# Optimization experiments

Hardware: AMD Instinct MI355X
Metric: run time of the kernel (lower is better)

Reference implementation:

```python
import jax, jax.numpy as jnp
import numpy as np

EPS = 1e-5

def _layernorm(x, g, b):
    m = jnp.mean(x, axis=-1, keepdims=True)
    v = jnp.var(x, axis=-1, keepdims=True)
    return (x - m) * jax.lax.rsqrt(v + EPS) * g + b

def setup_inputs() -> dict:
    key = jax.random.key(0)
    ks = jax.random.split(key, 8)
    B, N, D, H = 4, 2048, 1024, 16
    F = 2 * D
    s = 0.02
    return {
        "x": jax.random.normal(ks[0], (B, N, D), jnp.float32),
        "mask": jnp.zeros((B, N, N), jnp.float32),
        "Wq": jax.random.normal(ks[1], (D, D), jnp.float32) * s,
        "Wk": jax.random.normal(ks[2], (D, D), jnp.float32) * s,
        "Wv": jax.random.normal(ks[3], (D, D), jnp.float32) * s,
        "Wc": jax.random.normal(ks[4], (D, D), jnp.float32) * s,
        "bc": jnp.zeros((D,), jnp.float32),
        "W1": jax.random.normal(ks[5], (D, F), jnp.float32) * s,
        "b1": jnp.zeros((F,), jnp.float32),
        "W2": jax.random.normal(ks[6], (F, D), jnp.float32) * s,
        "b2": jnp.zeros((D,), jnp.float32),
        "g1": jnp.ones((D,), jnp.float32),
        "be1": jnp.zeros((D,), jnp.float32),
        "g2": jnp.ones((D,), jnp.float32),
        "be2": jnp.zeros((D,), jnp.float32),
    }

def reference(x, mask, Wq, Wk, Wv, Wc, bc, W1, b1, W2, b2, g1, be1, g2, be2):
    B, N, D = x.shape
    H = 16
    Dh = D // H
    scale = 1.0 / np.sqrt(Dh).astype(np.float32)
    # projections -> [B, H, N, Dh]
    def heads(t):
        return t.reshape(B, N, H, Dh).transpose(0, 2, 1, 3)
    q = heads(x @ Wq)
    k = heads(x @ Wk)
    v = heads(x @ Wv)
    score = jnp.einsum('bhnd,bhmd->bhnm', q, k) * scale + mask[:, None, :, :]
    attn = jnp.einsum('bhnm,bhmd->bhnd', jax.nn.softmax(score, axis=-1), v)
    attn = attn.transpose(0, 2, 1, 3).reshape(B, N, D)
    x = x + attn @ Wc + bc
    x = _layernorm(x, g1, be1)
    x = x + jnp.maximum(x @ W1 + b1, 0.0) @ W2 + b2
    x = _layernorm(x, g2, be2)
    return x
```

## Files before the change

### kernel.cpp

```cpp
#include <hip/hip_runtime.h>
#include <hip/hip_bf16.h>


#define DEV __device__ __forceinline__

using s16x8  = __attribute__((ext_vector_type(8))) short;
using f32x4  = __attribute__((ext_vector_type(4))) float;

DEV unsigned short f2bf(float f) {
  unsigned u = __float_as_uint(f);
  u += 0x7fffu + ((u >> 16) & 1u);
  return (unsigned short)(u >> 16);
}
DEV unsigned cvt_pk_bf16(float lo, float hi) {
  unsigned r;
  asm("v_cvt_pk_bf16_f32 %0, %1, %2" : "=v"(r) : "v"(lo), "v"(hi));
  return r;
}
DEV float bf2f(unsigned short b) { return __uint_as_float((unsigned)b << 16); }

typedef __attribute__((address_space(3))) unsigned lds_u32_t;
typedef const __attribute__((address_space(1))) unsigned glb_u32_t;

DEV void gld_lds16(const void* g, void* l) {
  __builtin_amdgcn_global_load_lds((glb_u32_t*)g, (lds_u32_t*)l, 16, 0, 0);
}

template<int RELU, int VOUT>
__global__ __launch_bounds__(512, 2)
void gemm8p(const unsigned short* __restrict__ A, const unsigned short* __restrict__ Bt,
            unsigned short* __restrict__ Cb, const float* __restrict__ bias,
            unsigned short* __restrict__ vtout, int M, int N, int K)
{
  __shared__ unsigned short Sh[2][2][256 * 64];
  const int tid = threadIdx.x;
  const int w = tid >> 6, lane = tid & 63;
  const int g = lane >> 4, q = lane & 15;
  const int wr = w >> 2, wc = w & 3;

  const int nwg  = gridDim.x * gridDim.y;
  const int flat = blockIdx.y * gridDim.x + blockIdx.x;
  const int rm   = (flat & 7) * (nwg >> 3) + (flat >> 3);
  const int m0 = (rm / gridDim.x) * 256, n0 = (rm % gridDim.x) * 256;

  f32x4 acc[8][4] = {};

  const int srow = w * 8 + (lane >> 3);
  const int scol = ((lane & 7) ^ (lane >> 3)) * 8;
  const unsigned short* Ag = A  + (size_t)(m0 + srow) * K + scol;
  const unsigned short* Bg = Bt + (size_t)(n0 + srow) * K + scol;

  auto STG = [&](const unsigned short* Gb, int buf, int ab, int half, int kt) {
    const unsigned short* gs = Gb + (size_t)(half * 128) * K + kt * 64;
    unsigned short* ls = &Sh[buf][ab][(half * 128 + w * 8) * 64];
    gld_lds16(gs, ls);
    gld_lds16(gs + (size_t)64 * K, ls + 64 * 64);
  };
  auto LDA = [&](int buf, int mq, s16x8 af[4][2]) {
#pragma unroll
    for (int mm = 0; mm < 4; ++mm) {
      const unsigned short* rp = &Sh[buf][0][(wr * 128 + mq * 64 + mm * 16 + q) * 64];
#pragma unroll
      for (int kk = 0; kk < 2; ++kk)
        af[mm][kk] = *(const s16x8*)(rp + (((kk * 4 + g) ^ (q & 7)) * 8));
    }
  };
  auto LDB = [&](int buf, int nq, s16x8 bf[2][2]) {
#pragma unroll
    for (int nn = 0; nn < 2; ++nn) {
      const unsigned short* rp = &Sh[buf][1][(wc * 64 + nq * 32 + nn * 16 + q) * 64];
#pragma unroll
      for (int kk = 0; kk < 2; ++kk)
        bf[nn][kk] = *(const s16x8*)(rp + (((kk * 4 + g) ^ (q & 7)) * 8));
    }
  };
  auto MQ = [&](int mq, int nq, const s16x8 af[4][2], const s16x8 bf[2][2]) {
    __builtin_amdgcn_s_setprio(1);
#pragma unroll
    for (int kk = 0; kk < 2; ++kk)
#pragma unroll
      for (int mm = 0; mm < 4; ++mm)
#pragma unroll
        for (int nn = 0; nn < 2; ++nn)
          acc[mq * 4 + mm][nq * 2 + nn] = __builtin_amdgcn_mfma_f32_16x16x32_bf16(
              af[mm][kk], bf[nn][kk], acc[mq * 4 + mm][nq * 2 + nn], 0, 0, 0);
    __builtin_amdgcn_s_setprio(0);
  };
  auto BAR = [&]() { __builtin_amdgcn_sched_barrier(0); __builtin_amdgcn_s_barrier(); };

  STG(Ag, 0, 0, 0, 0); STG(Ag, 0, 0, 1, 0);
  STG(Bg, 0, 1, 0, 0); STG(Bg, 0, 1, 1, 0);

  const int NKT = K >> 6;
  s16x8 af[4][2], bf0[2][2], bf1[2][2];
#pragma unroll 1
  for (int kt = 0; kt < NKT; ++kt) {
    const int b = kt & 1, sb = b ^ 1, kn = kt + 1;
    const bool stg = (kn < NKT);
    if (stg) { STG(Ag, sb, 0, 0, kn); asm volatile("s_waitcnt vmcnt(2)" ::: "memory"); }
    else     {                        asm volatile("s_waitcnt vmcnt(0)" ::: "memory"); }
    BAR();
    LDA(b, 0, af); LDB(b, 0, bf0);
    MQ(0, 0, af, bf0);
    BAR();
    if (stg) STG(Ag, sb, 0, 1, kn);
    LDB(b, 1, bf1);
    MQ(0, 1, af, bf1);
    BAR();
    if (stg) STG(Bg, sb, 1, 0, kn);
    LDA(b, 1, af);
    MQ(1, 0, af, bf0);
    BAR();
    if (stg) STG(Bg, sb, 1, 1, kn);
    MQ(1, 1, af, bf1);
    BAR();
  }

#pragma unroll
  for (int n = 0; n < 4; ++n) {
    const int col = n0 + wc * 64 + n * 16 + q;
    if (VOUT && col >= 2048) {
      const int cv = col - 2048;
#pragma unroll
      for (int m = 0; m < 8; ++m) {
        const int row0 = m0 + wr * 128 + m * 16 + g * 4;
        const int bb = row0 >> 11;
        ushort4 pk;
        pk.x = f2bf(acc[m][n][0]); pk.y = f2bf(acc[m][n][1]);
        pk.z = f2bf(acc[m][n][2]); pk.w = f2bf(acc[m][n][3]);
        *(ushort4*)(vtout + ((size_t)bb * 1024 + cv) * 2048 + (row0 & 2047)) = pk;
      }
    } else {
      const float scl = (VOUT && col < 1024) ? 0.18033688011112042f : 1.0f;
      const float bv = bias ? bias[col] : 0.0f;
#pragma unroll
      for (int m = 0; m < 8; ++m) {
        const int row0 = m0 + wr * 128 + m * 16 + g * 4;
#pragma unroll
        for (int r = 0; r < 4; ++r) {
          float v = acc[m][n][r] * scl + bv;
          if (RELU) v = fmaxf(v, 0.0f);
          Cb[(size_t)(row0 + r) * N + col] = f2bf(v);
        }
      }
    }
  }
}

template<int RELU, int RESID, int OUTF>
__global__ __launch_bounds__(256)
void gemm_bt(const unsigned short* __restrict__ A, const unsigned short* __restrict__ Bt,
             unsigned short* __restrict__ Cb, float* __restrict__ Cf,
             const float* __restrict__ bias, const float* __restrict__ resid,
             const unsigned short* __restrict__ residb,
             int M, int N, int K)
{
  __shared__ unsigned short As[2][4096];
  __shared__ unsigned short Bs[2][4096];
  const int tid  = threadIdx.x;
  const int wave = tid >> 6, lane = tid & 63;
  const int g = lane >> 4, q = lane & 15;

  const int nwg  = gridDim.x * gridDim.y;
  const int flat = blockIdx.y * gridDim.x + blockIdx.x;
  const int rm   = (nwg & 7) ? flat : ((flat & 7) * (nwg >> 3) + (flat >> 3));
  const int m0 = (rm / gridDim.x) * 128, n0 = (rm % gridDim.x) * 128;
  const int wr = wave >> 1, wc = wave & 1;

  f32x4 acc[4][4] = {};

  const int i0 = wave * 512 + lane * 8;
  const int i1 = 2048 + i0;

  auto STAGE = [&](int buf, int kt) {
    gld_lds16(A  + (size_t)(m0 + (i0 >> 5)) * K + kt + (i0 & 31), As[buf] + wave * 512);
    gld_lds16(Bt + (size_t)(n0 + (i0 >> 5)) * K + kt + (i0 & 31), Bs[buf] + wave * 512);
    gld_lds16(A  + (size_t)(m0 + (i1 >> 5)) * K + kt + (i1 & 31), As[buf] + 2048 + wave * 512);
    gld_lds16(Bt + (size_t)(n0 + (i1 >> 5)) * K + kt + (i1 & 31), Bs[buf] + 2048 + wave * 512);
  };

  STAGE(0, 0);
  __syncthreads();
  int cur = 0;
#pragma unroll 1
  for (int kt = 0; kt < K; kt += 32) {
    if (kt + 32 < K) STAGE(cur ^ 1, kt + 32);
    s16x8 a[4], b[4];
#pragma unroll
    for (int m = 0; m < 4; ++m)
      a[m] = *(const s16x8*)(As[cur] + (wr * 64 + m * 16 + q) * 32 + g * 8);
#pragma unroll
    for (int n = 0; n < 4; ++n)
      b[n] = *(const s16x8*)(Bs[cur] + (wc * 64 + n * 16 + q) * 32 + g * 8);
    __builtin_amdgcn_s_setprio(1);
#pragma unroll
    for (int m = 0; m < 4; ++m)
#pragma unroll
      for (int n = 0; n < 4; ++n)
        acc[m][n] = __builtin_amdgcn_mfma_f32_16x16x32_bf16(a[m], b[n], acc[m][n], 0, 0, 0);
    __builtin_amdgcn_s_setprio(0);
    __syncthreads();
    cur ^= 1;
  }

#pragma unroll
  for (int n = 0; n < 4; ++n) {
    const int col = n0 + wc * 64 + n * 16 + q;
    const float bv = bias ? bias[col] : 0.0f;
#pragma unroll
    for (int m = 0; m < 4; ++m) {
      const int row0 = m0 + wr * 64 + m * 16 + g * 4;
#pragma unroll
      for (int r = 0; r < 4; ++r) {
        float v = acc[m][n][r] + bv;
        if (RELU) v = fmaxf(v, 0.0f);
        if (RESID == 1) v += resid[(size_t)(row0 + r) * N + col];
        if (RESID == 2) v += bf2f(residb[(size_t)(row0 + r) * N + col]);
        if (OUTF) Cf[(size_t)(row0 + r) * N + col] = v;
        else      Cb[(size_t)(row0 + r) * N + col] = f2bf(v);
      }
    }
  }
}

__global__ __launch_bounds__(256, 4)
void attn_kernel(const unsigned short* __restrict__ qkv,
                 const unsigned short* __restrict__ vt,
                 const float* __restrict__ mask,
                 unsigned short* __restrict__ outb)
{
  __shared__ unsigned short Ks[2][4096];
  __shared__ unsigned short Vs[2][4096];
  __shared__ unsigned short Pl[4][1024];
  const int tid = threadIdx.x, wave = tid >> 6, lane = tid & 63;
  const int g = lane >> 4, q = lane & 15;

  const int flat = blockIdx.y * 32 + blockIdx.x;
  const int rm   = (flat & 7) * 256 + (flat >> 3);
  const int h  = rm & 15;
  const int qt = (rm >> 4) & 31;
  const int b  = rm >> 9;
  const int qrow = qt * 64 + wave * 16;
  const size_t tok0 = (size_t)b * 2048;

  const unsigned short* Qp = qkv + (tok0 + qrow + q) * 3072 + h * 64;
  const s16x8 bq0 = *(const s16x8*)(Qp + g * 8);
  const s16x8 bq1 = *(const s16x8*)(Qp + 32 + g * 8);
  const float* Mp = mask + ((size_t)b * 2048 + qrow + q) * 2048 + g * 4;

  const int lr = lane >> 3;
  const int sc = (lane & 7) ^ lr;
  const unsigned short* Kg = qkv + tok0 * 3072 + 1024 + h * 64
                           + (size_t)(wave * 16 + lr) * 3072 + sc * 8;
  const unsigned short* Vg = vt + (((size_t)b * 16 + h) * 64 + wave * 16 + lr) * 2048 + sc * 8;
  unsigned short* KsW = Ks[0] + wave * 1024;
  unsigned short* VsW = Vs[0] + wave * 1024;

  s16x8 ones;
#pragma unroll
  for (int j = 0; j < 8; ++j) ones[j] = (short)0x3F80;

  f32x4 ot[4] = {};
  f32x4 sacc = {};
  f32x4 mk0[4], mk1[4];
  char* Pw = (char*)&Pl[wave][0];
  const float L2E = 1.4426950408889634f;

  gld_lds16(Kg,            KsW);
  gld_lds16(Kg + 8 * 3072, KsW + 512);
  gld_lds16(Vg,            VsW);
  gld_lds16(Vg + 8 * 2048, VsW + 512);
#pragma unroll
  for (int m2 = 0; m2 < 4; ++m2) {
    const f32x4 r = *(const f32x4*)(Mp + m2 * 16);
#pragma unroll
    for (int i = 0; i < 4; ++i) mk0[m2][i] = fmaf(r[i], L2E, -8.0f);
  }
  __syncthreads();

#define ATTN_TILE(BUF, MKC, MKN, STG)                                          \
  {                                                                            \
    f32x4 mu[4];                                                               \
    if (STG) {                                                                 \
      Kg += 64 * 3072; Vg += 64; Mp += 64;                                     \
      gld_lds16(Kg,            KsW + (BUF ^ 1) * 4096);                        \
      gld_lds16(Kg + 8 * 3072, KsW + (BUF ^ 1) * 4096 + 512);                  \
      gld_lds16(Vg,            VsW + (BUF ^ 1) * 4096);                        \
      gld_lds16(Vg + 8 * 2048, VsW + (BUF ^ 1) * 4096 + 512);                  \
      mu[0] = *(const f32x4*)(Mp);      mu[1] = *(const f32x4*)(Mp + 16);      \
      mu[2] = *(const f32x4*)(Mp + 32); mu[3] = *(const f32x4*)(Mp + 48);      \
    }                                                                          \
    __builtin_amdgcn_s_setprio(1);                                             \
    _Pragma("unroll")                                                          \
    for (int m2 = 0; m2 < 4; ++m2) {                                           \
      const unsigned short* kp = Ks[BUF] + (m2 * 16 + q) * 64;                 \
      const s16x8 ak0 = *(const s16x8*)(kp + ((g       ^ (q & 7)) * 8));       \
      const s16x8 ak1 = *(const s16x8*)(kp + (((g + 4) ^ (q & 7)) * 8));       \
      MKC[m2] = __builtin_amdgcn_mfma_f32_16x16x32_bf16(ak0, bq0, MKC[m2], 0, 0, 0); \
      MKC[m2] = __builtin_amdgcn_mfma_f32_16x16x32_bf16(ak1, bq1, MKC[m2], 0, 0, 0); \
    }                                                                          \
    __builtin_amdgcn_s_setprio(0);                                             \
    _Pragma("unroll")                                                          \
    for (int m2 = 0; m2 < 4; ++m2) {                                           \
      MKC[m2][0] = exp2f(MKC[m2][0]); MKC[m2][1] = exp2f(MKC[m2][1]);          \
      MKC[m2][2] = exp2f(MKC[m2][2]); MKC[m2][3] = exp2f(MKC[m2][3]);          \
      const int bir  = m2 * 32 + g * 8;                                        \
      const int addr = q * 128 + (((bir >> 4) ^ (q & 7)) << 4) + (bir & 15);   \
      uint2 pk;                                                                \
      pk.x = cvt_pk_bf16(MKC[m2][0], MKC[m2][1]);                              \
      pk.y = cvt_pk_bf16(MKC[m2][2], MKC[m2][3]);                              \
      *(uint2*)(Pw + addr) = pk;                                               \
    }                                                                          \
    __builtin_amdgcn_s_setprio(1);                                             \
    _Pragma("unroll")                                                          \
    for (int kb = 0; kb < 2; ++kb) {                                           \
      const int blk = (kb * 4 + g) ^ (q & 7);                                  \
      const s16x8 pb = *(const s16x8*)(Pw + q * 128 + blk * 16);               \
      sacc = __builtin_amdgcn_mfma_f32_16x16x32_bf16(ones, pb, sacc, 0, 0, 0); \
      _Pragma("unroll")                                                        \
      for (int mm = 0; mm < 4; ++mm) {                                         \
        const s16x8 av = *(const s16x8*)(Vs[BUF] + (mm * 16 + q) * 64 + blk * 8); \
        ot[mm] = __builtin_amdgcn_mfma_f32_16x16x32_bf16(av, pb, ot[mm], 0, 0, 0); \
      }                                                                        \
    }                                                                          \
    __builtin_amdgcn_s_setprio(0);                                             \
    if (STG) {                                                                 \
      _Pragma("unroll")                                                        \
      for (int m2 = 0; m2 < 4; ++m2) {                                         \
        MKN[m2][0] = fmaf(mu[m2][0], L2E, -8.0f);                              \
        MKN[m2][1] = fmaf(mu[m2][1], L2E, -8.0f);                              \
        MKN[m2][2] = fmaf(mu[m2][2], L2E, -8.0f);                              \
        MKN[m2][3] = fmaf(mu[m2][3], L2E, -8.0f);                              \
      }                                                                        \
    }                                                                          \
    __syncthreads();                                                           \
  }

#pragma unroll 1
  for (int tt = 0; tt < 16; ++tt) {
    ATTN_TILE(0, mk0, mk1, true);
    ATTN_TILE(1, mk1, mk0, (tt < 15));
  }
#undef ATTN_TILE

  const float inv = 1.0f / sacc[0];
#pragma unroll
  for (int mm = 0; mm < 4; ++mm) {
    const int bir  = mm * 32 + g * 8;
    const int addr = q * 128 + (((bir >> 4) ^ (q & 7)) << 4) + (bir & 15);
    uint2 pk;
    pk.x = cvt_pk_bf16(ot[mm][0] * inv, ot[mm][1] * inv);
    pk.y = cvt_pk_bf16(ot[mm][2] * inv, ot[mm][3] * inv);
    *(uint2*)(Pw + addr) = pk;
  }
#pragma unroll
  for (int p = 0; p < 2; ++p) {
    const int c  = p * 64 + lane;
    const int qq = c >> 3, cc = c & 7;
    const int blk = cc ^ (qq & 7);
    const s16x8 vv = *(const s16x8*)(Pw + qq * 128 + blk * 16);
    *(s16x8*)(outb + (tok0 + qrow + qq) * 1024 + h * 64 + cc * 8) = vv;
  }
}

template<int INBF>
__global__ __launch_bounds__(256)
void ln_kernel(const float* __restrict__ inf, const unsigned short* __restrict__ inb,
               float* __restrict__ outf, unsigned short* __restrict__ outb,
               const float* __restrict__ gam, const float* __restrict__ bet)
{
  __shared__ float red[8];
  const int row = blockIdx.x, tid = threadIdx.x;
  f32x4 v;
  if (INBF) {
    const uint2 u = *(const uint2*)(inb + (size_t)row * 1024 + tid * 4);
    v[0] = __uint_as_float(u.x << 16); v[1] = __uint_as_float(u.x & 0xffff0000u);
    v[2] = __uint_as_float(u.y << 16); v[3] = __uint_as_float(u.y & 0xffff0000u);
  } else {
    v = *(const f32x4*)(inf + (size_t)row * 1024 + tid * 4);
  }
  float s  = v[0] + v[1] + v[2] + v[3];
  float ss = v[0]*v[0] + v[1]*v[1] + v[2]*v[2] + v[3]*v[3];
#pragma unroll
  for (int o = 1; o < 64; o <<= 1) { s += __shfl_xor(s, o); ss += __shfl_xor(ss, o); }
  if ((tid & 63) == 0) { red[tid >> 6] = s; red[4 + (tid >> 6)] = ss; }
  __syncthreads();
  s  = red[0] + red[1] + red[2] + red[3];
  ss = red[4] + red[5] + red[6] + red[7];
  const float mean = s * (1.0f / 1024.0f);
  const float var  = ss * (1.0f / 1024.0f) - mean * mean;
  const float rstd = rsqrtf(var + 1e-5f);
  const f32x4 gm = *(const f32x4*)(gam + tid * 4);
  const f32x4 bt = *(const f32x4*)(bet + tid * 4);
  f32x4 o;
#pragma unroll
  for (int j = 0; j < 4; ++j) o[j] = (v[j] - mean) * rstd * gm[j] + bt[j];
  if (outf) *(f32x4*)(outf + (size_t)row * 1024 + tid * 4) = o;
  if (outb) {
    uint2 pk; pk.x = cvt_pk_bf16(o[0], o[1]); pk.y = cvt_pk_bf16(o[2], o[3]);
    *(uint2*)(outb + (size_t)row * 1024 + tid * 4) = pk;
  }
}

__global__ __launch_bounds__(256)
void prep_kernel(const float* __restrict__ x, unsigned short* __restrict__ xb,
                 const float* __restrict__ Wq, const float* __restrict__ Wk,
                 const float* __restrict__ Wv, const float* __restrict__ Wc,
                 const float* __restrict__ W1, const float* __restrict__ W2,
                 unsigned short* __restrict__ wqkvt, unsigned short* __restrict__ wct,
                 unsigned short* __restrict__ w1t, unsigned short* __restrict__ w2t)
{
  const int bid = blockIdx.x;
  if (bid < 8192) {
    const size_t i = ((size_t)bid * 256 + threadIdx.x) * 4;
    const f32x4 v = *(const f32x4*)(x + i);
    uint2 pk; pk.x = cvt_pk_bf16(v[0], v[1]); pk.y = cvt_pk_bf16(v[2], v[3]);
    *(uint2*)(xb + i) = pk;
    return;
  }
  __shared__ float t[32][33];
  const int t2 = bid - 8192;
  const float* in; unsigned short* out; int R, C, bx, by;
  if (t2 < 4096) {
    const int widx = t2 >> 10, sub = t2 & 1023;
    in  = (widx == 0) ? Wq : (widx == 1) ? Wk : (widx == 2) ? Wv : Wc;
    out = (widx < 3) ? (wqkvt + (size_t)widx * 1024 * 1024) : wct;
    R = 1024; C = 1024; bx = sub & 31; by = sub >> 5;
  } else if (t2 < 6144) {
    const int sub = t2 - 4096;
    in = W1; out = w1t; R = 1024; C = 2048; bx = sub & 63; by = sub >> 6;
  } else {
    const int sub = t2 - 6144;
    in = W2; out = w2t; R = 2048; C = 1024; bx = sub & 31; by = sub >> 5;
  }
  const int tx = threadIdx.x & 31, ty = threadIdx.x >> 5;
  const int c0 = bx * 32, r0 = by * 32;
#pragma unroll
  for (int k = 0; k < 4; ++k)
    t[ty + k * 8][tx] = in[(size_t)(r0 + ty + k * 8) * C + c0 + tx];
  __syncthreads();
#pragma unroll
  for (int k = 0; k < 4; ++k)
    out[(size_t)(c0 + ty + k * 8) * R + r0 + tx] = f2bf(t[tx][ty + k * 8]);
}

extern "C" void kernel_launch(void* const* d_in, const int* in_sizes, int n_in,
                              void* d_out, int out_size, void* d_ws, size_t ws_size,
                              hipStream_t stream)
{
  (void)in_sizes; (void)n_in; (void)out_size; (void)ws_size;
  const float* x   = (const float*)d_in[0];
  const float* msk = (const float*)d_in[1];
  const float* Wq  = (const float*)d_in[2];
  const float* Wk  = (const float*)d_in[3];
  const float* Wv  = (const float*)d_in[4];
  const float* Wc  = (const float*)d_in[5];
  const float* bc  = (const float*)d_in[6];
  const float* W1  = (const float*)d_in[7];
  const float* b1  = (const float*)d_in[8];
  const float* W2  = (const float*)d_in[9];
  const float* b2  = (const float*)d_in[10];
  const float* g1  = (const float*)d_in[11];
  const float* be1 = (const float*)d_in[12];
  const float* g2  = (const float*)d_in[13];
  const float* be2 = (const float*)d_in[14];
  float* out = (float*)d_out;
  char* ws = (char*)d_ws;
  const size_t MB = 1u << 20;
  unsigned short* xb    = (unsigned short*)(ws + 0 * MB);
  unsigned short* wqkvt = (unsigned short*)(ws + 16 * MB);
  unsigned short* wct   = (unsigned short*)(ws + 22 * MB);
  unsigned short* w1t   = (unsigned short*)(ws + 24 * MB);
  unsigned short* w2t   = (unsigned short*)(ws + 28 * MB);
  unsigned short* qkv   = (unsigned short*)(ws + 32 * MB);
  unsigned short* vt    = (unsigned short*)(ws + 80 * MB);
  unsigned short* attnb = (unsigned short*)(ws + 96 * MB);
  unsigned short* y1b   = (unsigned short*)(ws + 112 * MB);
  unsigned short* h1b   = (unsigned short*)(ws + 128 * MB);
  unsigned short* midb  = (unsigned short*)(ws + 32 * MB);
  unsigned short* z2b   = (unsigned short*)(ws + 64 * MB);

  prep_kernel<<<16384, 256, 0, stream>>>(x, xb, Wq, Wk, Wv, Wc, W1, W2,
                                         wqkvt, wct, w1t, w2t);
  gemm8p<0, 1><<<dim3(12, 32), 512, 0, stream>>>(xb, wqkvt, qkv, nullptr, vt,
                                                 8192, 3072, 1024);
  attn_kernel<<<dim3(32, 64), 256, 0, stream>>>(qkv, vt, msk, attnb);
  gemm_bt<0, 2, 0><<<dim3(8, 64), 256, 0, stream>>>(attnb, wct, y1b, nullptr,
                                                    bc, nullptr, xb, 8192, 1024, 1024);
  ln_kernel<1><<<8192, 256, 0, stream>>>(nullptr, y1b, nullptr, h1b, g1, be1);
  gemm8p<1, 0><<<dim3(8, 32), 512, 0, stream>>>(h1b, w1t, midb, b1, nullptr,
                                                8192, 2048, 1024);
  gemm_bt<0, 2, 0><<<dim3(8, 64), 256, 0, stream>>>(midb, w2t, z2b, nullptr,
                                                    b2, nullptr, h1b, 8192, 1024, 2048);
  ln_kernel<1><<<8192, 256, 0, stream>>>(nullptr, z2b, out, nullptr, g2, be2);
}
```

Baseline: 407.2 us.

## Split-K the second FFN GEMM onto the 256-tile kernel, fuse reduction into LayerNorm

The W2 GEMM (K=2048, N=1024) moves from the smaller-tile gemm_bt kernel to the 256x256 gemm8p kernel with a two-way split over K. Each half writes fp32 partials, which gives 256 workgroups instead of 128 big tiles. The final LayerNorm now sums the two partials and adds bias and the bf16 residual before normalising, so the separate epilogue pass goes away. In exchange the code writes and reads two fp32 partial buffers of 32MB each, instead of one bf16 output.

```diff
diff --git a/kernel.cpp b/kernel.cpp
--- a/kernel.cpp
+++ b/kernel.cpp
@@ -26,11 +26,12 @@
   __builtin_amdgcn_global_load_lds((glb_u32_t*)g, (lds_u32_t*)l, 16, 0, 0);
 }
 
-template<int RELU, int VOUT>
+template<int RELU, int VOUT, int SPLITK>
 __global__ __launch_bounds__(512, 2)
 void gemm8p(const unsigned short* __restrict__ A, const unsigned short* __restrict__ Bt,
             unsigned short* __restrict__ Cb, const float* __restrict__ bias,
-            unsigned short* __restrict__ vtout, int M, int N, int K)
+            unsigned short* __restrict__ vtout, float* __restrict__ Cf,
+            int M, int N, int K)
 {
   __shared__ unsigned short Sh[2][2][256 * 64];
   const int tid = threadIdx.x;
@@ -41,14 +42,21 @@
   const int nwg  = gridDim.x * gridDim.y;
   const int flat = blockIdx.y * gridDim.x + blockIdx.x;
   const int rm   = (flat & 7) * (nwg >> 3) + (flat >> 3);
-  const int m0 = (rm / gridDim.x) * 256, n0 = (rm % gridDim.x) * 256;
+  int m0, n0, kz = 0;
+  if (SPLITK) {
+    kz = rm >> 7;
+    const int sp = rm & 127;
+    m0 = (sp >> 2) * 256; n0 = (sp & 3) * 256;
+  } else {
+    m0 = (rm / gridDim.x) * 256; n0 = (rm % gridDim.x) * 256;
+  }
 
   f32x4 acc[8][4] = {};
 
   const int srow = w * 8 + (lane >> 3);
   const int scol = ((lane & 7) ^ (lane >> 3)) * 8;
-  const unsigned short* Ag = A  + (size_t)(m0 + srow) * K + scol;
-  const unsigned short* Bg = Bt + (size_t)(n0 + srow) * K + scol;
+  const unsigned short* Ag = A  + (size_t)(m0 + srow) * K + scol + (SPLITK ? kz * (K >> 1) : 0);
+  const unsigned short* Bg = Bt + (size_t)(n0 + srow) * K + scol + (SPLITK ? kz * (K >> 1) : 0);
 
   auto STG = [&](const unsigned short* Gb, int buf, int ab, int half, int kt) {
     const unsigned short* gs = Gb + (size_t)(half * 128) * K + kt * 64;
@@ -91,7 +99,7 @@
   STG(Ag, 0, 0, 0, 0); STG(Ag, 0, 0, 1, 0);
   STG(Bg, 0, 1, 0, 0); STG(Bg, 0, 1, 1, 0);
 
-  const int NKT = K >> 6;
+  const int NKT = SPLITK ? (K >> 7) : (K >> 6);
   s16x8 af[4][2], bf0[2][2], bf1[2][2];
 #pragma unroll 1
   for (int kt = 0; kt < NKT; ++kt) {
@@ -119,7 +127,16 @@
 #pragma unroll
   for (int n = 0; n < 4; ++n) {
     const int col = n0 + wc * 64 + n * 16 + q;
-    if (VOUT && col >= 2048) {
+    if (SPLITK) {
+      float* Cp = Cf + (size_t)kz * M * N;
+#pragma unroll
+      for (int m = 0; m < 8; ++m) {
+        const int row0 = m0 + wr * 128 + m * 16 + g * 4;
+#pragma unroll
+        for (int r = 0; r < 4; ++r)
+          Cp[(size_t)(row0 + r) * N + col] = acc[m][n][r];
+      }
+    } else if (VOUT && col >= 2048) {
       const int cv = col - 2048;
 #pragma unroll
       for (int m = 0; m < 8; ++m) {
@@ -214,7 +231,6 @@
       for (int r = 0; r < 4; ++r) {
         float v = acc[m][n][r] + bv;
         if (RELU) v = fmaxf(v, 0.0f);
-        if (RESID == 1) v += resid[(size_t)(row0 + r) * N + col];
         if (RESID == 2) v += bf2f(residb[(size_t)(row0 + r) * N + col]);
         if (OUTF) Cf[(size_t)(row0 + r) * N + col] = v;
         else      Cb[(size_t)(row0 + r) * N + col] = f2bf(v);
@@ -363,21 +379,31 @@
   }
 }
 
-template<int INBF>
+template<int MODE>
 __global__ __launch_bounds__(256)
-void ln_kernel(const float* __restrict__ inf, const unsigned short* __restrict__ inb,
+void ln_kernel(const unsigned short* __restrict__ inb,
+               const float* __restrict__ p0, const float* __restrict__ p1,
+               const float* __restrict__ bias, const unsigned short* __restrict__ residb,
                float* __restrict__ outf, unsigned short* __restrict__ outb,
                const float* __restrict__ gam, const float* __restrict__ bet)
 {
   __shared__ float red[8];
   const int row = blockIdx.x, tid = threadIdx.x;
+  const size_t base = (size_t)row * 1024 + tid * 4;
   f32x4 v;
-  if (INBF) {
-    const uint2 u = *(const uint2*)(inb + (size_t)row * 1024 + tid * 4);
+  if (MODE == 0) {
+    const uint2 u = *(const uint2*)(inb + base);
     v[0] = __uint_as_float(u.x << 16); v[1] = __uint_as_float(u.x & 0xffff0000u);
     v[2] = __uint_as_float(u.y << 16); v[3] = __uint_as_float(u.y & 0xffff0000u);
   } else {
-    v = *(const f32x4*)(inf + (size_t)row * 1024 + tid * 4);
+    const f32x4 a = *(const f32x4*)(p0 + base);
+    const f32x4 c = *(const f32x4*)(p1 + base);
+    const f32x4 bs = *(const f32x4*)(bias + tid * 4);
+    const uint2 u = *(const uint2*)(residb + base);
+    v[0] = a[0] + c[0] + bs[0] + __uint_as_float(u.x << 16);
+    v[1] = a[1] + c[1] + bs[1] + __uint_as_float(u.x & 0xffff0000u);
+    v[2] = a[2] + c[2] + bs[2] + __uint_as_float(u.y << 16);
+    v[3] = a[3] + c[3] + bs[3] + __uint_as_float(u.y & 0xffff0000u);
   }
   float s  = v[0] + v[1] + v[2] + v[3];
   float ss = v[0]*v[0] + v[1]*v[1] + v[2]*v[2] + v[3]*v[3];
@@ -395,10 +421,10 @@
   f32x4 o;
 #pragma unroll
   for (int j = 0; j < 4; ++j) o[j] = (v[j] - mean) * rstd * gm[j] + bt[j];
-  if (outf) *(f32x4*)(outf + (size_t)row * 1024 + tid * 4) = o;
+  if (outf) *(f32x4*)(outf + base) = o;
   if (outb) {
     uint2 pk; pk.x = cvt_pk_bf16(o[0], o[1]); pk.y = cvt_pk_bf16(o[2], o[3]);
-    *(uint2*)(outb + (size_t)row * 1024 + tid * 4) = pk;
+    *(uint2*)(outb + base) = pk;
   }
 }
 
@@ -478,19 +504,21 @@
   unsigned short* y1b   = (unsigned short*)(ws + 112 * MB);
   unsigned short* h1b   = (unsigned short*)(ws + 128 * MB);
   unsigned short* midb  = (unsigned short*)(ws + 32 * MB);
-  unsigned short* z2b   = (unsigned short*)(ws + 64 * MB);
+  float*          pff   = (float*)(ws + 64 * MB);
 
   prep_kernel<<<16384, 256, 0, stream>>>(x, xb, Wq, Wk, Wv, Wc, W1, W2,
                                          wqkvt, wct, w1t, w2t);
-  gemm8p<0, 1><<<dim3(12, 32), 512, 0, stream>>>(xb, wqkvt, qkv, nullptr, vt,
-                                                 8192, 3072, 1024);
+  gemm8p<0, 1, 0><<<dim3(12, 32), 512, 0, stream>>>(xb, wqkvt, qkv, nullptr, vt,
+                                                    nullptr, 8192, 3072, 1024);
   attn_kernel<<<dim3(32, 64), 256, 0, stream>>>(qkv, vt, msk, attnb);
   gemm_bt<0, 2, 0><<<dim3(8, 64), 256, 0, stream>>>(attnb, wct, y1b, nullptr,
                                                     bc, nullptr, xb, 8192, 1024, 1024);
-  ln_kernel<1><<<8192, 256, 0, stream>>>(nullptr, y1b, nullptr, h1b, g1, be1);
-  gemm8p<1, 0><<<dim3(8, 32), 512, 0, stream>>>(h1b, w1t, midb, b1, nullptr,
-                                                8192, 2048, 1024);
-  gemm_bt<0, 2, 0><<<dim3(8, 64), 256, 0, stream>>>(midb, w2t, z2b, nullptr,
-                                                    b2, nullptr, h1b, 8192, 1024, 2048);
-  ln_kernel<1><<<8192, 256, 0, stream>>>(nullptr, z2b, out, nullptr, g2, be2);
-}
+  ln_kernel<0><<<8192, 256, 0, stream>>>(y1b, nullptr, nullptr, nullptr, nullptr,
+                                         nullptr, h1b, g1, be1);
+  gemm8p<1, 0, 0><<<dim3(8, 32), 512, 0, stream>>>(h1b, w1t, midb, b1, nullptr,
+                                                   nullptr, 8192, 2048, 1024);
+  gemm8p<0, 0, 1><<<dim3(8, 32), 512, 0, stream>>>(midb, w2t, nullptr, nullptr, nullptr,
+                                                   pff, 8192, 1024, 2048);
+  ln_kernel<1><<<8192, 256, 0, stream>>>(nullptr, pff, pff + (size_t)8192 * 1024,
+                                         b2, h1b, out, nullptr, g2, be2);
+}
```

Measured after the change: 403.1 us. About the same (-1.0%).
